# Performance work log

Hardware: AMD Instinct MI355X
Metric: run time of the kernel (lower is better)

## Reference

```python
import jax, jax.numpy as jnp
import numpy as np

NUM_HEADS = 10
LN_EPS = 1e-5

def setup_inputs() -> dict:
    key = jax.random.key(0)
    ks = jax.random.split(key, 8)
    B, H, N, D, Dt = 256, 200, 64, 640, 256
    s = 0.02
    return {
        'clicked_news': jax.random.normal(ks[0], (B, H, D), jnp.float32),
        'clicked_topics': jax.random.normal(ks[1], (B, H, Dt), jnp.float32),
        'cand_topics': jax.random.normal(ks[2], (B, N, Dt), jnp.float32),
        'Wq': jax.random.normal(ks[3], (D, Dt), jnp.float32) * s,
        'bq': jnp.zeros((D,), jnp.float32),
        'Wk': jax.random.normal(ks[4], (D, Dt), jnp.float32) * s,
        'bk': jnp.zeros((D,), jnp.float32),
        'Wv': jax.random.normal(ks[5], (D, D), jnp.float32) * s,
        'bv': jnp.zeros((D,), jnp.float32),
        'Wg': jax.random.normal(ks[6], (D, D), jnp.float32) * s,
        'bg': jnp.zeros((D,), jnp.float32),
        'ln_gamma': jnp.ones((D,), jnp.float32),
        'ln_beta': jnp.zeros((D,), jnp.float32),
    }

def reference(clicked_news, clicked_topics, cand_topics, Wq, bq, Wk, bk, Wv, bv, Wg, bg, ln_gamma, ln_beta):
    B, H, D = clicked_news.shape
    N = cand_topics.shape[1]
    nh = NUM_HEADS
    hd = D // nh
    scale = jnp.sqrt(jnp.asarray(D, clicked_news.dtype))

    Qf = cand_topics @ Wq.T + bq            # [B, N, D]
    Kf = clicked_topics @ Wk.T + bk         # [B, H, D]
    # V projection feeds `weighted`, which is dead code w.r.t. outputs; omitted.

    Q = Qf.reshape(B, N, nh, hd)
    K = Kf.reshape(B, H, nh, hd)
    scores = jnp.einsum('bnhd,bmhd->bhnm', Q, K) / scale   # [B, nh, N, H]
    attn = jax.nn.softmax(scores, axis=-1)                 # dropout is identity in eval

    # query weighting: softmax over candidates of ||Q||
    query_weights = jax.nn.softmax(jnp.linalg.norm(Qf, axis=-1), axis=1)   # [B, N]
    agg = (attn.sum(axis=1) * query_weights[:, :, None]).sum(axis=1)       # [B, H]
    attn_weights_agg = jax.nn.softmax(agg, axis=-1)                        # [B, H]

    weighted_clicked = attn_weights_agg[:, :, None] * clicked_news         # [B, H, D]
    gate = jax.nn.sigmoid(weighted_clicked @ Wg.T + bg)
    out = gate * weighted_clicked + (1.0 - gate) * clicked_news

    mu = out.mean(axis=-1, keepdims=True)
    var = out.var(axis=-1, keepdims=True)
    out = (out - mu) / jnp.sqrt(var + LN_EPS) * ln_gamma + ln_beta
    return out, attn_weights_agg
```

## Files before the change

### kernel.cpp

```cpp
#include <hip/hip_runtime.h>
#include <math.h>

#define B_  256
#define H_  200
#define N_  64
#define D_  640
#define DT_ 256
#define NH_ 10
#define HD_ 64
#define MT_ 13

typedef __attribute__((ext_vector_type(8))) short bf16x8;
typedef __attribute__((ext_vector_type(4))) float f32x4;

__device__ __forceinline__ float wave_reduce_sum(float v) {
    #pragma unroll
    for (int m = 32; m > 0; m >>= 1) v += __shfl_xor(v, m);
    return v;
}
__device__ __forceinline__ float wave_reduce_max(float v) {
    #pragma unroll
    for (int m = 32; m > 0; m >>= 1) v = fmaxf(v, __shfl_xor(v, m));
    return v;
}
__device__ __forceinline__ float red16_sum(float v) {
    #pragma unroll
    for (int m = 1; m < 16; m <<= 1) v += __shfl_xor(v, m);
    return v;
}
__device__ __forceinline__ float red16_max(float v) {
    #pragma unroll
    for (int m = 1; m < 16; m <<= 1) v = fmaxf(v, __shfl_xor(v, m));
    return v;
}
__device__ __forceinline__ short f2bf(float x) {
    unsigned u = __float_as_uint(x);
    unsigned r = (u + 0x7fffu + ((u >> 16) & 1u)) >> 16;
    return (short)r;
}
__device__ __forceinline__ float bf2f(short s) {
    return __uint_as_float(((unsigned)(unsigned short)s) << 16);
}
#define SWZ(row, byte) ((byte) ^ (((row) & 7) << 4))

__global__ __launch_bounds__(256) void convert_w(
    const float* __restrict__ src, short* __restrict__ dst, int n)
{
    for (int i = blockIdx.x * 256 + threadIdx.x; i < n; i += gridDim.x * 256)
        dst[i] = f2bf(src[i]);
}

__global__ __launch_bounds__(512, 2) void proj_mfma(
    const float* __restrict__ X, const short* __restrict__ Wb,
    const float* __restrict__ bias, short* __restrict__ Y)
{
    __shared__ short A_lds[64 * DT_];
    const int t = threadIdx.x;
    const int lane = t & 63, w = t >> 6;
    const int r16 = lane & 15, g = lane >> 4;
    const long row0 = (long)blockIdx.x * 64;

    {
        const int srow = t >> 3, sc = t & 7;
        const float4* src = (const float4*)(X + (row0 + srow) * DT_) + sc;
        float4 sv[8];
        #pragma unroll
        for (int j = 0; j < 8; ++j) sv[j] = src[8 * j];
        #pragma unroll
        for (int j = 0; j < 8; ++j) {
            short4 s;
            s.x = f2bf(sv[j].x); s.y = f2bf(sv[j].y);
            s.z = f2bf(sv[j].z); s.w = f2bf(sv[j].w);
            *(short4*)((char*)A_lds + SWZ(srow, srow * (DT_ * 2) + (sc + 8 * j) * 8)) = s;
        }
    }
    __syncthreads();

    f32x4 acc[5][4];
    #pragma unroll
    for (int ct = 0; ct < 5; ++ct)
        #pragma unroll
        for (int rt = 0; rt < 4; ++rt) acc[ct][rt] = (f32x4){0.f,0.f,0.f,0.f};

    const short* Wbase = Wb + (long)(w * 80 + r16) * DT_ + g * 8;

    bf16x8 aA[4], bA[5], aB[4], bB[5];
    #pragma unroll
    for (int rt = 0; rt < 4; ++rt) {
        const int row = rt * 16 + r16;
        aA[rt] = *(const bf16x8*)((const char*)A_lds + SWZ(row, row * (DT_ * 2) + g * 16));
    }
    #pragma unroll
    for (int ct = 0; ct < 5; ++ct) bA[ct] = *(const bf16x8*)(Wbase + ct * 16 * DT_);

    #pragma unroll
    for (int kc = 0; kc < 8; kc += 2) {
        {
            const int kn = kc + 1;
            #pragma unroll
            for (int rt = 0; rt < 4; ++rt) {
                const int row = rt * 16 + r16;
                aB[rt] = *(const bf16x8*)((const char*)A_lds +
                          SWZ(row, row * (DT_ * 2) + kn * 64 + g * 16));
            }
            #pragma unroll
            for (int ct = 0; ct < 5; ++ct)
                bB[ct] = *(const bf16x8*)(Wbase + ct * 16 * DT_ + kn * 32);
        }
        #pragma unroll
        for (int ct = 0; ct < 5; ++ct)
            #pragma unroll
            for (int rt = 0; rt < 4; ++rt)
                acc[ct][rt] = __builtin_amdgcn_mfma_f32_16x16x32_bf16(
                                  aA[rt], bA[ct], acc[ct][rt], 0, 0, 0);
        {
            const int kn = (kc + 2 < 8) ? kc + 2 : 0;
            #pragma unroll
            for (int rt = 0; rt < 4; ++rt) {
                const int row = rt * 16 + r16;
                aA[rt] = *(const bf16x8*)((const char*)A_lds +
                          SWZ(row, row * (DT_ * 2) + kn * 64 + g * 16));
            }
            #pragma unroll
            for (int ct = 0; ct < 5; ++ct)
                bA[ct] = *(const bf16x8*)(Wbase + ct * 16 * DT_ + kn * 32);
        }
        #pragma unroll
        for (int ct = 0; ct < 5; ++ct)
            #pragma unroll
            for (int rt = 0; rt < 4; ++rt)
                acc[ct][rt] = __builtin_amdgcn_mfma_f32_16x16x32_bf16(
                                  aB[rt], bB[ct], acc[ct][rt], 0, 0, 0);
    }

    #pragma unroll
    for (int ct = 0; ct < 5; ++ct) {
        const int col = w * 80 + ct * 16 + r16;
        const float bv = bias[col];
        #pragma unroll
        for (int rt = 0; rt < 4; ++rt)
            #pragma unroll
            for (int i = 0; i < 4; ++i)
                Y[(row0 + rt * 16 + g * 4 + i) * (long)D_ + col] =
                    f2bf(acc[ct][rt][i] + bv);
    }
}

__global__ __launch_bounds__(512, 2) void attn2(
    const short* __restrict__ Qb, const short* __restrict__ Kb,
    float* __restrict__ aw, float* __restrict__ out_tail)
{
    __shared__ float qn_l[N_];
    __shared__ float qw_l[N_];
    __shared__ float aggp[8][MT_ * 16];
    __shared__ float red2[2];
    const int t = threadIdx.x;
    const int lane = t & 63, w = t >> 6;
    const int wm = w & 3, hh = w >> 2;
    const int r16 = lane & 15, g = lane >> 4;
    const int b = blockIdx.x;

    if (hh == 0) {
        const short* qrow = Qb + ((long)(b * N_ + wm * 16 + r16)) * D_ + g * 160;
        float ss = 0.f;
        #pragma unroll
        for (int j = 0; j < 20; ++j) {
            bf16x8 v = *(const bf16x8*)(qrow + j * 8);
            #pragma unroll
            for (int e = 0; e < 8; ++e) { float f = bf2f(v[e]); ss += f * f; }
        }
        ss += __shfl_xor(ss, 16);
        ss += __shfl_xor(ss, 32);
        if (g == 0) qn_l[wm * 16 + r16] = ss;
    }
    __syncthreads();
    if (w == 0) {
        float v = sqrtf(qn_l[lane]);
        float mx = wave_reduce_max(v);
        float e = __expf(v - mx);
        float s = wave_reduce_sum(e);
        qw_l[lane] = e / s;
    }
    __syncthreads();

    float qwr[4];
    #pragma unroll
    for (int i = 0; i < 4; ++i) qwr[i] = qw_l[wm * 16 + g * 4 + i];

    const float inv_scale = 0.0395284707521047f;
    float aggl[MT_];
    #pragma unroll
    for (int mt = 0; mt < MT_; ++mt) aggl[mt] = 0.f;

    for (int hi = 0; hi < 5; ++hi) {
        const int h = hh * 5 + hi;
        const short* qbase = Qb + ((long)(b * N_ + wm * 16 + r16)) * D_ + h * HD_ + g * 8;
        bf16x8 a0 = *(const bf16x8*)(qbase);
        bf16x8 a1 = *(const bf16x8*)(qbase + 32);
        bf16x8 kb0[MT_], kb1[MT_];
        #pragma unroll
        for (int mt = 0; mt < MT_; ++mt) {
            const short* kbase = Kb + ((long)(b * H_ + mt * 16 + r16)) * D_ + h * HD_ + g * 8;
            kb0[mt] = *(const bf16x8*)(kbase);
            kb1[mt] = *(const bf16x8*)(kbase + 32);
        }
        f32x4 acc[MT_];
        #pragma unroll
        for (int mt = 0; mt < MT_; ++mt) {
            f32x4 z = {0.f,0.f,0.f,0.f};
            z = __builtin_amdgcn_mfma_f32_16x16x32_bf16(a0, kb0[mt], z, 0, 0, 0);
            z = __builtin_amdgcn_mfma_f32_16x16x32_bf16(a1, kb1[mt], z, 0, 0, 0);
            acc[mt] = z;
        }
        const bool tailok = (r16 < 8);
        float mx[4] = {-INFINITY, -INFINITY, -INFINITY, -INFINITY};
        #pragma unroll
        for (int mt = 0; mt < MT_; ++mt) {
            const bool valid = (mt < 12) || tailok;
            #pragma unroll
            for (int i = 0; i < 4; ++i)
                if (valid) mx[i] = fmaxf(mx[i], acc[mt][i]);
        }
        #pragma unroll
        for (int i = 0; i < 4; ++i) mx[i] = red16_max(mx[i]);
        float sum[4] = {0.f, 0.f, 0.f, 0.f};
        #pragma unroll
        for (int mt = 0; mt < MT_; ++mt) {
            const bool valid = (mt < 12) || tailok;
            #pragma unroll
            for (int i = 0; i < 4; ++i) {
                float e = valid ? __expf((acc[mt][i] - mx[i]) * inv_scale) : 0.f;
                acc[mt][i] = e;
                sum[i] += e;
            }
        }
        float fct[4];
        #pragma unroll
        for (int i = 0; i < 4; ++i) fct[i] = qwr[i] / red16_sum(sum[i]);
        #pragma unroll
        for (int mt = 0; mt < MT_; ++mt)
            aggl[mt] += acc[mt][0] * fct[0] + acc[mt][1] * fct[1]
                      + acc[mt][2] * fct[2] + acc[mt][3] * fct[3];
    }
    #pragma unroll
    for (int mt = 0; mt < MT_; ++mt) {
        aggl[mt] += __shfl_xor(aggl[mt], 16);
        aggl[mt] += __shfl_xor(aggl[mt], 32);
    }
    if (g == 0) {
        #pragma unroll
        for (int mt = 0; mt < MT_; ++mt) aggp[w][mt * 16 + r16] = aggl[mt];
    }
    __syncthreads();
    if (t < MT_ * 16) {
        float v = 0.f;
        #pragma unroll
        for (int j = 0; j < 8; ++j) v += aggp[j][t];
        aggp[0][t] = v;
    }
    __syncthreads();
    if (w == 0) {
        float v0 = aggp[0][lane], v1 = aggp[0][lane + 64], v2 = aggp[0][lane + 128];
        const bool has3 = lane < (H_ - 192);
        float v3 = has3 ? aggp[0][lane + 192] : -INFINITY;
        float mx = wave_reduce_max(fmaxf(fmaxf(v0, v1), fmaxf(v2, v3)));
        float s = __expf(v0 - mx) + __expf(v1 - mx) + __expf(v2 - mx)
                + (has3 ? __expf(v3 - mx) : 0.f);
        s = wave_reduce_sum(s);
        if (lane == 0) { red2[0] = mx; red2[1] = s; }
    }
    __syncthreads();
    if (t < H_) {
        float v = __expf(aggp[0][t] - red2[0]) / red2[1];
        aw[b * H_ + t] = v;
        out_tail[b * H_ + t] = v;
    }
}

__global__ __launch_bounds__(512, 2) void out_mfma(
    const float* __restrict__ clicked, const float* __restrict__ aw,
    const short* __restrict__ Wgb, const float* __restrict__ bg,
    const float* __restrict__ gamma, const float* __restrict__ beta,
    float* __restrict__ out)
{
    __shared__ short A_lds[64 * D_];
    const int t = threadIdx.x;
    const int lane = t & 63, w = t >> 6;
    const int r16 = lane & 15, g = lane >> 4;
    const long row0 = (long)blockIdx.x * 64;

    {
        const int srow = t >> 3, sc = t & 7;
        const float a = aw[row0 + srow];
        const float4* src = (const float4*)(clicked + (row0 + srow) * D_) + sc;
        float4 sv[20];
        #pragma unroll
        for (int j = 0; j < 20; ++j) sv[j] = src[8 * j];
        #pragma unroll
        for (int j = 0; j < 20; ++j) {
            short4 s;
            s.x = f2bf(sv[j].x * a); s.y = f2bf(sv[j].y * a);
            s.z = f2bf(sv[j].z * a); s.w = f2bf(sv[j].w * a);
            *(short4*)((char*)A_lds + SWZ(srow, srow * (D_ * 2) + (sc + 8 * j) * 8)) = s;
        }
    }
    __syncthreads();

    f32x4 acc[5][4];
    #pragma unroll
    for (int ct = 0; ct < 5; ++ct)
        #pragma unroll
        for (int rt = 0; rt < 4; ++rt) acc[ct][rt] = (f32x4){0.f,0.f,0.f,0.f};

    const short* Wbase = Wgb + (long)(w * 80 + r16) * D_ + g * 8;

    bf16x8 aA[4], bA[5], aB[4], bB[5];
    #pragma unroll
    for (int rt = 0; rt < 4; ++rt) {
        const int row = rt * 16 + r16;
        aA[rt] = *(const bf16x8*)((const char*)A_lds + SWZ(row, row * (D_ * 2) + g * 16));
    }
    #pragma unroll
    for (int ct = 0; ct < 5; ++ct) bA[ct] = *(const bf16x8*)(Wbase + ct * 16 * D_);

    #pragma unroll
    for (int kc = 0; kc < 20; kc += 2) {
        {
            const int kn = kc + 1;
            #pragma unroll
            for (int rt = 0; rt < 4; ++rt) {
                const int row = rt * 16 + r16;
                aB[rt] = *(const bf16x8*)((const char*)A_lds +
                          SWZ(row, row * (D_ * 2) + kn * 64 + g * 16));
            }
            #pragma unroll
            for (int ct = 0; ct < 5; ++ct)
                bB[ct] = *(const bf16x8*)(Wbase + ct * 16 * D_ + kn * 32);
        }
        #pragma unroll
        for (int ct = 0; ct < 5; ++ct)
            #pragma unroll
            for (int rt = 0; rt < 4; ++rt)
                acc[ct][rt] = __builtin_amdgcn_mfma_f32_16x16x32_bf16(
                                  aA[rt], bA[ct], acc[ct][rt], 0, 0, 0);
        {
            const int kn = (kc + 2 < 20) ? kc + 2 : 0;
            #pragma unroll
            for (int rt = 0; rt < 4; ++rt) {
                const int row = rt * 16 + r16;
                aA[rt] = *(const bf16x8*)((const char*)A_lds +
                          SWZ(row, row * (D_ * 2) + kn * 64 + g * 16));
            }
            #pragma unroll
            for (int ct = 0; ct < 5; ++ct)
                bA[ct] = *(const bf16x8*)(Wbase + ct * 16 * D_ + kn * 32);
        }
        #pragma unroll
        for (int ct = 0; ct < 5; ++ct)
            #pragma unroll
            for (int rt = 0; rt < 4; ++rt)
                acc[ct][rt] = __builtin_amdgcn_mfma_f32_16x16x32_bf16(
                                  aB[rt], bB[ct], acc[ct][rt], 0, 0, 0);
    }
    __syncthreads();

    #pragma unroll
    for (int ct = 0; ct < 5; ++ct) {
        const int col = w * 80 + ct * 16 + r16;
        const float bv = bg[col];
        #pragma unroll
        for (int rt = 0; rt < 4; ++rt)
            #pragma unroll
            for (int i = 0; i < 4; ++i) {
                const int row = rt * 16 + g * 4 + i;
                *(short*)((char*)A_lds + SWZ(row, row * (D_ * 2) + col * 2)) =
                    f2bf(acc[ct][rt][i] + bv);
            }
    }
    __syncthreads();

    for (int rr = 0; rr < 8; ++rr) {
        const int r = w * 8 + rr;
        const long base = (row0 + r) * (long)D_;
        const float aww = aw[row0 + r];
        float cl[10], ov[10];
        #pragma unroll
        for (int i = 0; i < 10; ++i) cl[i] = clicked[base + lane + 64 * i];
        float s = 0.f, sq = 0.f;
        #pragma unroll
        for (int i = 0; i < 10; ++i) {
            const int c = lane + 64 * i;
            float z = bf2f(*(const short*)((const char*)A_lds +
                           SWZ(r, r * (D_ * 2) + c * 2)));
            float gt = 1.f / (1.f + __expf(-z));
            float o  = gt * (aww * cl[i]) + (1.f - gt) * cl[i];
            ov[i] = o; s += o; sq += o * o;
        }
        s  = wave_reduce_sum(s);
        sq = wave_reduce_sum(sq);
        const float mu  = s * (1.f / D_);
        const float var = sq * (1.f / D_) - mu * mu;
        const float rinv = 1.0f / sqrtf(var + 1e-5f);
        #pragma unroll
        for (int i = 0; i < 10; ++i) {
            const int c = lane + 64 * i;
            out[base + c] = (ov[i] - mu) * rinv * gamma[c] + beta[c];
        }
    }
}

extern "C" void kernel_launch(void* const* d_in, const int* in_sizes, int n_in,
                              void* d_out, int out_size, void* d_ws, size_t ws_size,
                              hipStream_t stream) {
    const float* clicked_news   = (const float*)d_in[0];
    const float* clicked_topics = (const float*)d_in[1];
    const float* cand_topics    = (const float*)d_in[2];
    const float* Wq = (const float*)d_in[3];
    const float* bq = (const float*)d_in[4];
    const float* Wk = (const float*)d_in[5];
    const float* bk = (const float*)d_in[6];
    const float* Wg = (const float*)d_in[9];
    const float* bg = (const float*)d_in[10];
    const float* ln_gamma = (const float*)d_in[11];
    const float* ln_beta  = (const float*)d_in[12];

    float* out = (float*)d_out;
    float* ws  = (float*)d_ws;

    float* aw = ws;
    short* sbase = (short*)(ws + (long)B_ * H_);
    short* Qb   = sbase;
    short* Wq_b = Qb + (long)B_ * N_ * D_;
    short* Wg_b = Wq_b + (long)D_ * DT_;
    short* Wk_b = Wg_b + (long)D_ * D_;
    short* Kb = (short*)d_out;
    float* out_tail = out + (long)B_ * H_ * D_;

    convert_w<<<128, 256, 0, stream>>>(Wq, Wq_b, D_ * DT_);
    convert_w<<<128, 256, 0, stream>>>(Wk, Wk_b, D_ * DT_);
    convert_w<<<256, 256, 0, stream>>>(Wg, Wg_b, D_ * D_);

    proj_mfma<<<(B_ * N_) / 64, 512, 0, stream>>>(cand_topics, Wq_b, bq, Qb);
    proj_mfma<<<(B_ * H_) / 64, 512, 0, stream>>>(clicked_topics, Wk_b, bk, Kb);
    attn2<<<B_, 512, 0, stream>>>(Qb, Kb, aw, out_tail);
    out_mfma<<<(B_ * H_) / 64, 512, 0, stream>>>(clicked_news, aw, Wg_b, bg,
                                                 ln_gamma, ln_beta, out);
}
```

Measured before the change: 311.6 us.

## Fuse gate and LayerNorm epilogue into registers, halve out_mfma row tile

The output kernel now stages clicked_news unscaled as bf16 in LDS and applies the attention weight after the GEMM, using the identity (a·x)W = a·(xW). The gate, blend and LayerNorm run directly on the MFMA accumulators, with per-row sums reduced across waves through LDS. This removes the second global read of clicked_news and the LDS round-trip of the gate logits. Tiles shrink to 32 rows with a launch bound of 4 blocks per SM to raise occupancy, at the cost of reloading Wg more often. The blend now uses bf16-rounded clicked values instead of fp32, which adds some precision error.

```diff
diff --git a/kernel.cpp b/kernel.cpp
--- a/kernel.cpp
+++ b/kernel.cpp
@@ -277,49 +277,60 @@
     }
 }
 
-__global__ __launch_bounds__(512, 2) void out_mfma(
+__global__ __launch_bounds__(512, 4) void out_mfma(
     const float* __restrict__ clicked, const float* __restrict__ aw,
     const short* __restrict__ Wgb, const float* __restrict__ bg,
     const float* __restrict__ gamma, const float* __restrict__ beta,
     float* __restrict__ out)
 {
-    __shared__ short A_lds[64 * D_];
+    __shared__ short A_lds[32 * D_];
+    __shared__ float bg_l[D_];
+    __shared__ float gm_l[D_];
+    __shared__ float bt_l[D_];
+    __shared__ float aw_l[32];
+    __shared__ float part[32][8][2];
+    __shared__ float mu_l[32], ri_l[32];
     const int t = threadIdx.x;
     const int lane = t & 63, w = t >> 6;
     const int r16 = lane & 15, g = lane >> 4;
-    const long row0 = (long)blockIdx.x * 64;
+    const long row0 = (long)blockIdx.x * 32;
+
+    for (int i = t; i < D_; i += 512) {
+        bg_l[i] = bg[i]; gm_l[i] = gamma[i]; bt_l[i] = beta[i];
+    }
+    if (t < 32) aw_l[t] = aw[row0 + t];
 
     {
-        const int srow = t >> 3, sc = t & 7;
-        const float a = aw[row0 + srow];
+        const int srow = t >> 4, sc = t & 15;
         const float4* src = (const float4*)(clicked + (row0 + srow) * D_) + sc;
-        float4 sv[20];
-        #pragma unroll
-        for (int j = 0; j < 20; ++j) sv[j] = src[8 * j];
-        #pragma unroll
-        for (int j = 0; j < 20; ++j) {
-            short4 s;
-            s.x = f2bf(sv[j].x * a); s.y = f2bf(sv[j].y * a);
-            s.z = f2bf(sv[j].z * a); s.w = f2bf(sv[j].w * a);
-            *(short4*)((char*)A_lds + SWZ(srow, srow * (D_ * 2) + (sc + 8 * j) * 8)) = s;
-        }
-    }
-    __syncthreads();
-
-    f32x4 acc[5][4];
-    #pragma unroll
-    for (int ct = 0; ct < 5; ++ct)
-        #pragma unroll
-        for (int rt = 0; rt < 4; ++rt) acc[ct][rt] = (f32x4){0.f,0.f,0.f,0.f};
+        #pragma unroll
+        for (int batch = 0; batch < 2; ++batch) {
+            float4 sv[5];
+            #pragma unroll
+            for (int j = 0; j < 5; ++j) sv[j] = src[16 * (batch * 5 + j)];
+            #pragma unroll
+            for (int j = 0; j < 5; ++j) {
+                const int jj = batch * 5 + j;
+                short4 s;
+                s.x = f2bf(sv[j].x); s.y = f2bf(sv[j].y);
+                s.z = f2bf(sv[j].z); s.w = f2bf(sv[j].w);
+                *(short4*)((char*)A_lds +
+                    SWZ(srow, srow * (D_ * 2) + (sc + 16 * jj) * 8)) = s;
+            }
+        }
+    }
+    __syncthreads();
+
+    f32x4 acc[5][2];
+    #pragma unroll
+    for (int ct = 0; ct < 5; ++ct) {
+        acc[ct][0] = (f32x4){0.f,0.f,0.f,0.f};
+        acc[ct][1] = (f32x4){0.f,0.f,0.f,0.f};
+    }
 
     const short* Wbase = Wgb + (long)(w * 80 + r16) * D_ + g * 8;
 
-    bf16x8 aA[4], bA[5], aB[4], bB[5];
-    #pragma unroll
-    for (int rt = 0; rt < 4; ++rt) {
-        const int row = rt * 16 + r16;
-        aA[rt] = *(const bf16x8*)((const char*)A_lds + SWZ(row, row * (D_ * 2) + g * 16));
-    }
+    bf16x8 bA[5], bB[5];
     #pragma unroll
     for (int ct = 0; ct < 5; ++ct) bA[ct] = *(const bf16x8*)(Wbase + ct * 16 * D_);
 
@@ -327,85 +338,103 @@
     for (int kc = 0; kc < 20; kc += 2) {
         {
             const int kn = kc + 1;
-            #pragma unroll
-            for (int rt = 0; rt < 4; ++rt) {
-                const int row = rt * 16 + r16;
-                aB[rt] = *(const bf16x8*)((const char*)A_lds +
-                          SWZ(row, row * (D_ * 2) + kn * 64 + g * 16));
-            }
             #pragma unroll
             for (int ct = 0; ct < 5; ++ct)
                 bB[ct] = *(const bf16x8*)(Wbase + ct * 16 * D_ + kn * 32);
         }
-        #pragma unroll
-        for (int ct = 0; ct < 5; ++ct)
-            #pragma unroll
-            for (int rt = 0; rt < 4; ++rt)
-                acc[ct][rt] = __builtin_amdgcn_mfma_f32_16x16x32_bf16(
-                                  aA[rt], bA[ct], acc[ct][rt], 0, 0, 0);
+        {
+            bf16x8 a0 = *(const bf16x8*)((const char*)A_lds +
+                         SWZ(r16, r16 * (D_ * 2) + kc * 64 + g * 16));
+            const int row1 = 16 + r16;
+            bf16x8 a1 = *(const bf16x8*)((const char*)A_lds +
+                         SWZ(row1, row1 * (D_ * 2) + kc * 64 + g * 16));
+            #pragma unroll
+            for (int ct = 0; ct < 5; ++ct) {
+                acc[ct][0] = __builtin_amdgcn_mfma_f32_16x16x32_bf16(a0, bA[ct], acc[ct][0], 0, 0, 0);
+                acc[ct][1] = __builtin_amdgcn_mfma_f32_16x16x32_bf16(a1, bA[ct], acc[ct][1], 0, 0, 0);
+            }
+        }
         {
             const int kn = (kc + 2 < 20) ? kc + 2 : 0;
-            #pragma unroll
-            for (int rt = 0; rt < 4; ++rt) {
-                const int row = rt * 16 + r16;
-                aA[rt] = *(const bf16x8*)((const char*)A_lds +
-                          SWZ(row, row * (D_ * 2) + kn * 64 + g * 16));
-            }
             #pragma unroll
             for (int ct = 0; ct < 5; ++ct)
                 bA[ct] = *(const bf16x8*)(Wbase + ct * 16 * D_ + kn * 32);
         }
-        #pragma unroll
-        for (int ct = 0; ct < 5; ++ct)
-            #pragma unroll
-            for (int rt = 0; rt < 4; ++rt)
-                acc[ct][rt] = __builtin_amdgcn_mfma_f32_16x16x32_bf16(
-                                  aB[rt], bB[ct], acc[ct][rt], 0, 0, 0);
-    }
-    __syncthreads();
+        {
+            const int kn = kc + 1;
+            bf16x8 a0 = *(const bf16x8*)((const char*)A_lds +
+                         SWZ(r16, r16 * (D_ * 2) + kn * 64 + g * 16));
+            const int row1 = 16 + r16;
+            bf16x8 a1 = *(const bf16x8*)((const char*)A_lds +
+                         SWZ(row1, row1 * (D_ * 2) + kn * 64 + g * 16));
+            #pragma unroll
+            for (int ct = 0; ct < 5; ++ct) {
+                acc[ct][0] = __builtin_amdgcn_mfma_f32_16x16x32_bf16(a0, bB[ct], acc[ct][0], 0, 0, 0);
+                acc[ct][1] = __builtin_amdgcn_mfma_f32_16x16x32_bf16(a1, bB[ct], acc[ct][1], 0, 0, 0);
+            }
+        }
+    }
+
+    float psum[2][4], psq[2][4];
+    #pragma unroll
+    for (int rt = 0; rt < 2; ++rt)
+        #pragma unroll
+        for (int i = 0; i < 4; ++i) { psum[rt][i] = 0.f; psq[rt][i] = 0.f; }
 
     #pragma unroll
     for (int ct = 0; ct < 5; ++ct) {
         const int col = w * 80 + ct * 16 + r16;
-        const float bv = bg[col];
-        #pragma unroll
-        for (int rt = 0; rt < 4; ++rt)
+        const float bgv = bg_l[col];
+        #pragma unroll
+        for (int rt = 0; rt < 2; ++rt)
             #pragma unroll
             for (int i = 0; i < 4; ++i) {
                 const int row = rt * 16 + g * 4 + i;
-                *(short*)((char*)A_lds + SWZ(row, row * (D_ * 2) + col * 2)) =
-                    f2bf(acc[ct][rt][i] + bv);
-            }
-    }
-    __syncthreads();
-
-    for (int rr = 0; rr < 8; ++rr) {
-        const int r = w * 8 + rr;
-        const long base = (row0 + r) * (long)D_;
-        const float aww = aw[row0 + r];
-        float cl[10], ov[10];
-        #pragma unroll
-        for (int i = 0; i < 10; ++i) cl[i] = clicked[base + lane + 64 * i];
-        float s = 0.f, sq = 0.f;
-        #pragma unroll
-        for (int i = 0; i < 10; ++i) {
-            const int c = lane + 64 * i;
-            float z = bf2f(*(const short*)((const char*)A_lds +
-                           SWZ(r, r * (D_ * 2) + c * 2)));
-            float gt = 1.f / (1.f + __expf(-z));
-            float o  = gt * (aww * cl[i]) + (1.f - gt) * cl[i];
-            ov[i] = o; s += o; sq += o * o;
-        }
-        s  = wave_reduce_sum(s);
-        sq = wave_reduce_sum(sq);
-        const float mu  = s * (1.f / D_);
-        const float var = sq * (1.f / D_) - mu * mu;
-        const float rinv = 1.0f / sqrtf(var + 1e-5f);
-        #pragma unroll
-        for (int i = 0; i < 10; ++i) {
-            const int c = lane + 64 * i;
-            out[base + c] = (ov[i] - mu) * rinv * gamma[c] + beta[c];
-        }
+                const float awr = aw_l[row];
+                const float cl = bf2f(*(const short*)((const char*)A_lds +
+                                   SWZ(row, row * (D_ * 2) + col * 2)));
+                const float z  = awr * acc[ct][rt][i] + bgv;
+                const float gt = 1.f / (1.f + __expf(-z));
+                const float o  = cl * (1.f + gt * (awr - 1.f));
+                acc[ct][rt][i] = o;
+                psum[rt][i] += o; psq[rt][i] += o * o;
+            }
+    }
+    #pragma unroll
+    for (int rt = 0; rt < 2; ++rt)
+        #pragma unroll
+        for (int i = 0; i < 4; ++i) {
+            const float s  = red16_sum(psum[rt][i]);
+            const float sq = red16_sum(psq[rt][i]);
+            if (r16 == 0) {
+                part[rt * 16 + g * 4 + i][w][0] = s;
+                part[rt * 16 + g * 4 + i][w][1] = sq;
+            }
+        }
+    __syncthreads();
+    if (t < 32) {
+        float s = 0.f, q = 0.f;
+        #pragma unroll
+        for (int j = 0; j < 8; ++j) { s += part[t][j][0]; q += part[t][j][1]; }
+        const float m = s * (1.f / D_);
+        const float v = q * (1.f / D_) - m * m;
+        mu_l[t] = m;
+        ri_l[t] = 1.0f / sqrtf(v + 1e-5f);
+    }
+    __syncthreads();
+
+    #pragma unroll
+    for (int ct = 0; ct < 5; ++ct) {
+        const int col = w * 80 + ct * 16 + r16;
+        const float gmv = gm_l[col], btv = bt_l[col];
+        #pragma unroll
+        for (int rt = 0; rt < 2; ++rt)
+            #pragma unroll
+            for (int i = 0; i < 4; ++i) {
+                const int row = rt * 16 + g * 4 + i;
+                out[(row0 + row) * (long)D_ + col] =
+                    (acc[ct][rt][i] - mu_l[row]) * ri_l[row] * gmv + btv;
+            }
     }
 }
 
@@ -443,6 +472,6 @@
     proj_mfma<<<(B_ * N_) / 64, 512, 0, stream>>>(cand_topics, Wq_b, bq, Qb);
     proj_mfma<<<(B_ * H_) / 64, 512, 0, stream>>>(clicked_topics, Wk_b, bk, Kb);
     attn2<<<B_, 512, 0, stream>>>(Qb, Kb, aw, out_tail);
-    out_mfma<<<(B_ * H_) / 64, 512, 0, stream>>>(clicked_news, aw, Wg_b, bg,
+    out_mfma<<<(B_ * H_) / 32, 512, 0, stream>>>(clicked_news, aw, Wg_b, bg,
                                                  ln_gamma, ln_beta, out);
 }
```

Result: slower. 347.2 us (+11.4%).

## Factor attention weight out of gate GEMM and split into tiled GEMM plus blend-LN

Applied to the files above, without the earlier changes.

The gate GEMM is computed on raw clicked_news, and the per-row attention weight is applied afterwards to the output, since (a*x)W = a*(xW). This lets the GEMM run as a standalone tiled 128x128 kernel that loads fp32 A and bf16 W straight into LDS with global_load_lds. A separate blend+LayerNorm kernel reads Z back and applies the gate and normalization. The work is done in two halves so Z fits in the workspace, at the cost of an extra Z round trip through global memory and more launches.

```diff
diff --git a/kernel.cpp b/kernel.cpp
--- a/kernel.cpp
+++ b/kernel.cpp
@@ -9,6 +9,7 @@
 #define NH_ 10
 #define HD_ 64
 #define MT_ 13
+#define MH_ 25600
 
 typedef __attribute__((ext_vector_type(8))) short bf16x8;
 typedef __attribute__((ext_vector_type(4))) float f32x4;
@@ -42,6 +43,12 @@
     return __uint_as_float(((unsigned)(unsigned short)s) << 16);
 }
 #define SWZ(row, byte) ((byte) ^ (((row) & 7) << 4))
+
+__device__ __forceinline__ void gload_lds16(const void* g, void* lds) {
+    __builtin_amdgcn_global_load_lds(
+        (const __attribute__((address_space(1))) void*)g,
+        (__attribute__((address_space(3))) void*)lds, 16, 0, 0);
+}
 
 __global__ __launch_bounds__(256) void convert_w(
     const float* __restrict__ src, short* __restrict__ dst, int n)
@@ -277,135 +284,117 @@
     }
 }
 
-__global__ __launch_bounds__(512, 2) void out_mfma(
-    const float* __restrict__ clicked, const float* __restrict__ aw,
-    const short* __restrict__ Wgb, const float* __restrict__ bg,
+__global__ __launch_bounds__(256, 3) void zgemm(
+    const float* __restrict__ A, const short* __restrict__ Wb,
+    short* __restrict__ Z)
+{
+    __shared__ float A_f[128 * 64];
+    __shared__ short B_lds[128 * 64];
+    const int t = threadIdx.x;
+    const int lane = t & 63, w = t >> 6;
+    const int wm = w >> 1, wn = w & 1;
+    const int r16 = lane & 15, g = lane >> 4;
+    const int row0 = (blockIdx.x / 5) * 128;
+    const int col0 = (blockIdx.x % 5) * 128;
+
+    f32x4 acc[4][4];
+    #pragma unroll
+    for (int ct = 0; ct < 4; ++ct)
+        #pragma unroll
+        for (int rt = 0; rt < 4; ++rt) acc[ct][rt] = (f32x4){0.f,0.f,0.f,0.f};
+
+    for (int k = 0; k < 10; ++k) {
+        const int k0 = k * 64;
+        #pragma unroll
+        for (int j = 0; j < 8; ++j) {
+            const int u = t + j * 256;
+            const int row = u >> 4, gr = u & 15;
+            gload_lds16(A + (long)(row0 + row) * D_ + k0 + gr * 4,
+                        (char*)A_f + u * 16);
+        }
+        #pragma unroll
+        for (int j = 0; j < 4; ++j) {
+            const int u = t + j * 256;
+            const int col = u >> 3, gr = u & 7;
+            gload_lds16(Wb + (long)(col0 + col) * D_ + k0 + gr * 8,
+                        (char*)B_lds + u * 16);
+        }
+        __syncthreads();
+
+        #pragma unroll
+        for (int kk = 0; kk < 2; ++kk) {
+            bf16x8 a[4];
+            #pragma unroll
+            for (int rt = 0; rt < 4; ++rt) {
+                const int row = wm * 64 + rt * 16 + r16;
+                float4 f0 = *(const float4*)(A_f + row * 64 + kk * 32 + g * 8);
+                float4 f1 = *(const float4*)(A_f + row * 64 + kk * 32 + g * 8 + 4);
+                bf16x8 av;
+                av[0] = f2bf(f0.x); av[1] = f2bf(f0.y); av[2] = f2bf(f0.z); av[3] = f2bf(f0.w);
+                av[4] = f2bf(f1.x); av[5] = f2bf(f1.y); av[6] = f2bf(f1.z); av[7] = f2bf(f1.w);
+                a[rt] = av;
+            }
+            bf16x8 b[4];
+            #pragma unroll
+            for (int ct = 0; ct < 4; ++ct) {
+                const int col = wn * 64 + ct * 16 + r16;
+                b[ct] = *(const bf16x8*)(B_lds + col * 64 + kk * 32 + g * 8);
+            }
+            #pragma unroll
+            for (int ct = 0; ct < 4; ++ct)
+                #pragma unroll
+                for (int rt = 0; rt < 4; ++rt)
+                    acc[ct][rt] = __builtin_amdgcn_mfma_f32_16x16x32_bf16(
+                                      a[rt], b[ct], acc[ct][rt], 0, 0, 0);
+        }
+        __syncthreads();
+    }
+
+    #pragma unroll
+    for (int ct = 0; ct < 4; ++ct) {
+        const int col = col0 + wn * 64 + ct * 16 + r16;
+        #pragma unroll
+        for (int rt = 0; rt < 4; ++rt)
+            #pragma unroll
+            for (int i = 0; i < 4; ++i)
+                Z[(long)(row0 + wm * 64 + rt * 16 + g * 4 + i) * D_ + col] =
+                    f2bf(acc[ct][rt][i]);
+    }
+}
+
+__global__ __launch_bounds__(256) void blendln(
+    const float* __restrict__ cl, const short* __restrict__ Z,
+    const float* __restrict__ aw, const float* __restrict__ bg,
     const float* __restrict__ gamma, const float* __restrict__ beta,
     float* __restrict__ out)
 {
-    __shared__ short A_lds[64 * D_];
     const int t = threadIdx.x;
     const int lane = t & 63, w = t >> 6;
-    const int r16 = lane & 15, g = lane >> 4;
-    const long row0 = (long)blockIdx.x * 64;
-
-    {
-        const int srow = t >> 3, sc = t & 7;
-        const float a = aw[row0 + srow];
-        const float4* src = (const float4*)(clicked + (row0 + srow) * D_) + sc;
-        float4 sv[20];
-        #pragma unroll
-        for (int j = 0; j < 20; ++j) sv[j] = src[8 * j];
-        #pragma unroll
-        for (int j = 0; j < 20; ++j) {
-            short4 s;
-            s.x = f2bf(sv[j].x * a); s.y = f2bf(sv[j].y * a);
-            s.z = f2bf(sv[j].z * a); s.w = f2bf(sv[j].w * a);
-            *(short4*)((char*)A_lds + SWZ(srow, srow * (D_ * 2) + (sc + 8 * j) * 8)) = s;
-        }
-    }
-    __syncthreads();
-
-    f32x4 acc[5][4];
-    #pragma unroll
-    for (int ct = 0; ct < 5; ++ct)
-        #pragma unroll
-        for (int rt = 0; rt < 4; ++rt) acc[ct][rt] = (f32x4){0.f,0.f,0.f,0.f};
-
-    const short* Wbase = Wgb + (long)(w * 80 + r16) * D_ + g * 8;
-
-    bf16x8 aA[4], bA[5], aB[4], bB[5];
-    #pragma unroll
-    for (int rt = 0; rt < 4; ++rt) {
-        const int row = rt * 16 + r16;
-        aA[rt] = *(const bf16x8*)((const char*)A_lds + SWZ(row, row * (D_ * 2) + g * 16));
-    }
-    #pragma unroll
-    for (int ct = 0; ct < 5; ++ct) bA[ct] = *(const bf16x8*)(Wbase + ct * 16 * D_);
-
-    #pragma unroll
-    for (int kc = 0; kc < 20; kc += 2) {
-        {
-            const int kn = kc + 1;
-            #pragma unroll
-            for (int rt = 0; rt < 4; ++rt) {
-                const int row = rt * 16 + r16;
-                aB[rt] = *(const bf16x8*)((const char*)A_lds +
-                          SWZ(row, row * (D_ * 2) + kn * 64 + g * 16));
-            }
-            #pragma unroll
-            for (int ct = 0; ct < 5; ++ct)
-                bB[ct] = *(const bf16x8*)(Wbase + ct * 16 * D_ + kn * 32);
-        }
-        #pragma unroll
-        for (int ct = 0; ct < 5; ++ct)
-            #pragma unroll
-            for (int rt = 0; rt < 4; ++rt)
-                acc[ct][rt] = __builtin_amdgcn_mfma_f32_16x16x32_bf16(
-                                  aA[rt], bA[ct], acc[ct][rt], 0, 0, 0);
-        {
-            const int kn = (kc + 2 < 20) ? kc + 2 : 0;
-            #pragma unroll
-            for (int rt = 0; rt < 4; ++rt) {
-                const int row = rt * 16 + r16;
-                aA[rt] = *(const bf16x8*)((const char*)A_lds +
-                          SWZ(row, row * (D_ * 2) + kn * 64 + g * 16));
-            }
-            #pragma unroll
-            for (int ct = 0; ct < 5; ++ct)
-                bA[ct] = *(const bf16x8*)(Wbase + ct * 16 * D_ + kn * 32);
-        }
-        #pragma unroll
-        for (int ct = 0; ct < 5; ++ct)
-            #pragma unroll
-            for (int rt = 0; rt < 4; ++rt)
-                acc[ct][rt] = __builtin_amdgcn_mfma_f32_16x16x32_bf16(
-                                  aB[rt], bB[ct], acc[ct][rt], 0, 0, 0);
-    }
-    __syncthreads();
-
-    #pragma unroll
-    for (int ct = 0; ct < 5; ++ct) {
-        const int col = w * 80 + ct * 16 + r16;
-        const float bv = bg[col];
-        #pragma unroll
-        for (int rt = 0; rt < 4; ++rt)
-            #pragma unroll
-            for (int i = 0; i < 4; ++i) {
-                const int row = rt * 16 + g * 4 + i;
-                *(short*)((char*)A_lds + SWZ(row, row * (D_ * 2) + col * 2)) =
-                    f2bf(acc[ct][rt][i] + bv);
-            }
-    }
-    __syncthreads();
-
-    for (int rr = 0; rr < 8; ++rr) {
-        const int r = w * 8 + rr;
-        const long base = (row0 + r) * (long)D_;
-        const float aww = aw[row0 + r];
-        float cl[10], ov[10];
-        #pragma unroll
-        for (int i = 0; i < 10; ++i) cl[i] = clicked[base + lane + 64 * i];
-        float s = 0.f, sq = 0.f;
-        #pragma unroll
-        for (int i = 0; i < 10; ++i) {
-            const int c = lane + 64 * i;
-            float z = bf2f(*(const short*)((const char*)A_lds +
-                           SWZ(r, r * (D_ * 2) + c * 2)));
-            float gt = 1.f / (1.f + __expf(-z));
-            float o  = gt * (aww * cl[i]) + (1.f - gt) * cl[i];
-            ov[i] = o; s += o; sq += o * o;
-        }
-        s  = wave_reduce_sum(s);
-        sq = wave_reduce_sum(sq);
-        const float mu  = s * (1.f / D_);
-        const float var = sq * (1.f / D_) - mu * mu;
-        const float rinv = 1.0f / sqrtf(var + 1e-5f);
-        #pragma unroll
-        for (int i = 0; i < 10; ++i) {
-            const int c = lane + 64 * i;
-            out[base + c] = (ov[i] - mu) * rinv * gamma[c] + beta[c];
-        }
+    const int row = blockIdx.x * 4 + w;
+    const float awr = aw[row];
+    const long base = (long)row * D_;
+
+    float o[10];
+    float s = 0.f, sq = 0.f;
+    #pragma unroll
+    for (int i = 0; i < 10; ++i) {
+        const int col = lane + 64 * i;
+        const float y = bf2f(Z[base + col]);
+        const float c = cl[base + col];
+        const float z = awr * y + bg[col];
+        const float gt = 1.f / (1.f + __expf(-z));
+        const float ov = c * (1.f + gt * (awr - 1.f));
+        o[i] = ov; s += ov; sq += ov * ov;
+    }
+    s  = wave_reduce_sum(s);
+    sq = wave_reduce_sum(sq);
+    const float mu  = s * (1.f / D_);
+    const float var = sq * (1.f / D_) - mu * mu;
+    const float ri  = 1.0f / sqrtf(var + 1e-5f);
+    #pragma unroll
+    for (int i = 0; i < 10; ++i) {
+        const int col = lane + 64 * i;
+        out[base + col] = (o[i] - mu) * ri * gamma[col] + beta[col];
     }
 }
 
@@ -427,12 +416,12 @@
     float* out = (float*)d_out;
     float* ws  = (float*)d_ws;
 
-    float* aw = ws;
-    short* sbase = (short*)(ws + (long)B_ * H_);
-    short* Qb   = sbase;
-    short* Wq_b = Qb + (long)B_ * N_ * D_;
-    short* Wg_b = Wq_b + (long)D_ * DT_;
-    short* Wk_b = Wg_b + (long)D_ * D_;
+    float* aw   = ws;
+    short* Wq_b = (short*)(aw + (long)B_ * H_);
+    short* Wk_b = Wq_b + (long)D_ * DT_;
+    short* Wg_b = Wk_b + (long)D_ * DT_;
+    short* Qb   = Wg_b + (long)D_ * D_;
+    short* Z    = Qb;
     short* Kb = (short*)d_out;
     float* out_tail = out + (long)B_ * H_ * D_;
 
@@ -443,6 +432,13 @@
     proj_mfma<<<(B_ * N_) / 64, 512, 0, stream>>>(cand_topics, Wq_b, bq, Qb);
     proj_mfma<<<(B_ * H_) / 64, 512, 0, stream>>>(clicked_topics, Wk_b, bk, Kb);
     attn2<<<B_, 512, 0, stream>>>(Qb, Kb, aw, out_tail);
-    out_mfma<<<(B_ * H_) / 64, 512, 0, stream>>>(clicked_news, aw, Wg_b, bg,
-                                                 ln_gamma, ln_beta, out);
-}
+
+    for (int h = 0; h < 2; ++h) {
+        const long off = (long)h * MH_;
+        zgemm<<<(MH_ / 128) * 5, 256, 0, stream>>>(
+            clicked_news + off * D_, Wg_b, Z);
+        blendln<<<MH_ / 4, 256, 0, stream>>>(
+            clicked_news + off * D_, Z, aw + off, bg, ln_gamma, ln_beta,
+            out + off * D_);
+    }
+}
```

Result: slower. 333.6 us (+7.1%).
